# Optimization experiments

Measured on AMD Instinct MI355X. Metric: run time of the kernel, lower is better.

## Reference

```python
import jax, jax.numpy as jnp
import numpy as np

D_MODEL = 1024
N_HEADS = 16
N_GROUPS = 4
CONTEXT_LEN = 512
D_H = D_MODEL // N_HEADS          # 64
GROUP_SIZE = N_HEADS // N_GROUPS  # 4
B, S = 4, 2048


def setup_inputs() -> dict:
    key = jax.random.key(0)
    ks = jax.random.split(key, 9)
    s = 0.02
    return {
        "x": jax.random.normal(ks[0], (B, S, D_MODEL), dtype=jnp.float32),
        "Wq": jax.random.normal(ks[1], (D_MODEL, D_MODEL), dtype=jnp.float32) * s,
        "bq": jax.random.normal(ks[2], (D_MODEL,), dtype=jnp.float32) * s,
        "Wk": jax.random.normal(ks[3], (D_MODEL, N_GROUPS * D_H), dtype=jnp.float32) * s,
        "bk": jax.random.normal(ks[4], (N_GROUPS * D_H,), dtype=jnp.float32) * s,
        "Wv": jax.random.normal(ks[5], (D_MODEL, N_GROUPS * D_H), dtype=jnp.float32) * s,
        "bv": jax.random.normal(ks[6], (N_GROUPS * D_H,), dtype=jnp.float32) * s,
        "Wo": jax.random.normal(ks[7], (D_MODEL, D_MODEL), dtype=jnp.float32) * s,
        "bo": jax.random.normal(ks[8], (D_MODEL,), dtype=jnp.float32) * s,
    }


def reference(x, Wq, bq, Wk, bk, Wv, bv, Wo, bo):
    b, s = x.shape[0], x.shape[1]
    # Projections. q: [b, n_groups, group_size, s, d_h]; k/v: [b, n_groups, s, d_h]
    q = (x @ Wq + bq).reshape(b, s, N_GROUPS, GROUP_SIZE, D_H)
    q = jnp.transpose(q, (0, 2, 3, 1, 4))
    k = jnp.transpose((x @ Wk + bk).reshape(b, s, N_GROUPS, D_H), (0, 2, 1, 3))
    v = jnp.transpose((x @ Wv + bv).reshape(b, s, N_GROUPS, D_H), (0, 2, 1, 3))
    # Grouped scores (einsum broadcast == repeat_interleave of k over group_size)
    scores = jnp.einsum("bghqd,bgkd->bghqk", q, k) / jnp.sqrt(jnp.float32(D_H))
    # Sliding-window causal mask (cached_len == s when use_cache=False)
    i = jnp.arange(s)
    j = jnp.arange(s)
    upper = (i - CONTEXT_LEN)[:, None] >= j[None, :]   # too-old keys
    lower = i[:, None] < j[None, :]                    # future keys
    mask = upper | lower                               # [s, s]
    scores = jnp.where(mask, jnp.float32(-1e9), scores)
    att = jax.nn.softmax(scores, axis=-1)
    out = jnp.einsum("bghqk,bgkd->bghqd", att, v)      # [b, g, h, s, d_h]
    out = jnp.transpose(out, (0, 3, 1, 2, 4)).reshape(b, s, D_MODEL)
    return out @ Wo + bo
```

## Files before the change

### kernel.cpp

```cpp
#include <hip/hip_runtime.h>
#include <cstdint>
#include <cstddef>

typedef __attribute__((ext_vector_type(8))) short short8;
typedef __attribute__((ext_vector_type(4))) short short4v;
typedef __attribute__((ext_vector_type(4))) float f32x4;
typedef __attribute__((ext_vector_type(4))) unsigned short ushort4v;
typedef unsigned short ushort_t;

union Frag8 { short4v h[2]; short8 v; };
union PFrag { unsigned int w[4]; short8 v; };

__device__ __forceinline__ ushort_t f2bf(float f) {
  unsigned int u = __builtin_bit_cast(unsigned int, f);
  u += 0x7FFFu + ((u >> 16) & 1u);
  return (ushort_t)(u >> 16);
}

__device__ __forceinline__ void gload16(const void* g, void* l) {
  __builtin_amdgcn_global_load_lds(
      (const __attribute__((address_space(1))) unsigned int*)g,
      (__attribute__((address_space(3))) unsigned int*)l, 16, 0, 0);
}

__global__ void cast_x_kernel(const float* __restrict__ x, ushort_t* __restrict__ o) {
  int i = (blockIdx.x * 256 + threadIdx.x) * 4;
  const float4 v = *reinterpret_cast<const float4*>(x + i);
  ushort4v r = { f2bf(v.x), f2bf(v.y), f2bf(v.z), f2bf(v.w) };
  *reinterpret_cast<ushort4v*>(o + i) = r;
}

__global__ __launch_bounds__(256) void transpose_w_kernel(
    const float* __restrict__ Wq, const float* __restrict__ Wk,
    const float* __restrict__ Wv, const float* __restrict__ Wo,
    ushort_t* __restrict__ Wt) {
  __shared__ float tile[32][33];
  const int tn = blockIdx.x, tk = blockIdx.y;
  const int n0 = tn * 32;
  const float* W; int ldn, nloc;
  if      (n0 < 1024) { W = Wq; ldn = 1024; nloc = n0; }
  else if (n0 < 1280) { W = Wk; ldn = 256;  nloc = n0 - 1024; }
  else if (n0 < 1536) { W = Wv; ldn = 256;  nloc = n0 - 1280; }
  else                { W = Wo; ldn = 1024; nloc = n0 - 1536; }
  const int t = threadIdx.x;
  const int sr = t >> 3, sc = (t & 7) * 4;
  const float4 v = *reinterpret_cast<const float4*>(W + (size_t)(tk * 32 + sr) * ldn + nloc + sc);
  tile[sr][sc] = v.x; tile[sr][sc + 1] = v.y; tile[sr][sc + 2] = v.z; tile[sr][sc + 3] = v.w;
  __syncthreads();
  const int wr = t >> 3, wc = (t & 7) * 4;
  ushort4v o = { f2bf(tile[wc][wr]), f2bf(tile[wc + 1][wr]),
                 f2bf(tile[wc + 2][wr]), f2bf(tile[wc + 3][wr]) };
  *reinterpret_cast<ushort4v*>(Wt + (size_t)(n0 + wr) * 1024 + tk * 32 + wc) = o;
}

__global__ void prep_bias_kernel(const float* __restrict__ bq, const float* __restrict__ bk,
                                 const float* __restrict__ bv, float* __restrict__ bqkv) {
  int t = blockIdx.x * 256 + threadIdx.x;
  if (t < 1536) bqkv[t] = (t < 1024) ? bq[t] : (t < 1280) ? bk[t - 1024] : bv[t - 1280];
}

#define GEMM_IDS \
  const int tid = threadIdx.x;                        \
  const int w = tid >> 6, lane = tid & 63;            \
  const int wm = w >> 1, wn = w & 1;                  \
  const int g = lane >> 4, r16 = lane & 15;

#define GEMM_KLOOP(APTR, BPTR)                                                          \
  const f32x4 vzero = {0.f, 0.f, 0.f, 0.f};                                             \
  f32x4 acc[4][4];                                                                      \
  _Pragma("unroll") for (int i = 0; i < 4; ++i)                                         \
    _Pragma("unroll") for (int j = 0; j < 4; ++j) acc[i][j] = vzero;                    \
  auto stage = [&](int s, int k0) {                                                     \
    char* base = LdsB + s * 16384;                                                      \
    _Pragma("unroll") for (int i = 0; i < 2; ++i) {                                     \
      const int u = tid + i * 256;                                                      \
      const int row = u >> 2;                                                           \
      const int pu = (u & 3) ^ ((u >> 3) & 3);                                          \
      gload16((const char*)(APTR) + (size_t)(bm * 128 + row) * 2048 + k0 * 2 + pu * 16, \
              base + u * 16);                                                           \
    }                                                                                   \
    _Pragma("unroll") for (int i = 0; i < 2; ++i) {                                     \
      const int u = tid + i * 256;                                                      \
      const int row = u >> 2;                                                           \
      const int pu = (u & 3) ^ ((u >> 3) & 3);                                          \
      gload16((const char*)(BPTR) + (size_t)(bn * 128 + row) * 2048 + k0 * 2 + pu * 16, \
              base + 8192 + u * 16);                                                    \
    }                                                                                   \
  };                                                                                    \
  stage(0, 0);                                                                          \
  stage(1, 32);                                                                         \
  const int fsw = (g ^ ((r16 >> 1) & 3)) << 4;                                          \
  for (int t = 0; t < 32; ++t) {                                                        \
    if (t < 31) { asm volatile("s_waitcnt vmcnt(4) lgkmcnt(0)" ::: "memory"); }         \
    else        { asm volatile("s_waitcnt vmcnt(0) lgkmcnt(0)" ::: "memory"); }         \
    __builtin_amdgcn_s_barrier();                                                       \
    if (t + 2 < 32) stage((t + 2) % 3, (t + 2) * 32);                                   \
    const char* Ab = LdsB + (t % 3) * 16384;                                            \
    const char* Bb = Ab + 8192;                                                         \
    short8 af[4], bf[4];                                                                \
    _Pragma("unroll") for (int mi = 0; mi < 4; ++mi)                                    \
      af[mi] = *(const short8*)(Ab + (wm * 64 + mi * 16 + r16) * 64 + fsw);             \
    _Pragma("unroll") for (int ni = 0; ni < 4; ++ni)                                    \
      bf[ni] = *(const short8*)(Bb + (wn * 64 + ni * 16 + r16) * 64 + fsw);             \
    __builtin_amdgcn_s_setprio(1);                                                      \
    _Pragma("unroll") for (int mi = 0; mi < 4; ++mi)                                    \
      _Pragma("unroll") for (int ni = 0; ni < 4; ++ni)                                  \
        acc[mi][ni] = __builtin_amdgcn_mfma_f32_16x16x32_bf16(af[mi], bf[ni], acc[mi][ni], 0, 0, 0); \
    __builtin_amdgcn_s_setprio(0);                                                      \
  }

__global__ __launch_bounds__(256, 3) void gemm_qkv_kernel(
    const ushort_t* __restrict__ A, const ushort_t* __restrict__ Bt,
    const float* __restrict__ bias,
    ushort_t* __restrict__ Qb, ushort_t* __restrict__ Kb, ushort_t* __restrict__ Vt)
{
  __shared__ __align__(16) char LdsB[49152];
  const int xcd = blockIdx.x & 7, ii = blockIdx.x >> 3;
  const int bm = xcd * 8 + ii / 12, bn = ii % 12;
  GEMM_IDS
  GEMM_KLOOP(A, Bt)

  float bcol[4];
#pragma unroll
  for (int ni = 0; ni < 4; ++ni) bcol[ni] = bias[bn * 128 + wn * 64 + ni * 16 + r16];
  if (bn < 8) {
#pragma unroll
    for (int mi = 0; mi < 4; ++mi)
#pragma unroll
      for (int ni = 0; ni < 4; ++ni) {
        const int col = bn * 128 + wn * 64 + ni * 16 + r16;
#pragma unroll
        for (int rr = 0; rr < 4; ++rr) {
          const int row = bm * 128 + wm * 64 + mi * 16 + g * 4 + rr;
          Qb[(size_t)row * 1024 + col] = f2bf((acc[mi][ni][rr] + bcol[ni]) * 0.180336881f);
        }
      }
  } else if (bn < 10) {
#pragma unroll
    for (int mi = 0; mi < 4; ++mi)
#pragma unroll
      for (int ni = 0; ni < 4; ++ni) {
        const int c = bn * 128 + wn * 64 + ni * 16 + r16 - 1024;
        const int gi = c >> 6, dd = c & 63;
#pragma unroll
        for (int rr = 0; rr < 4; ++rr) {
          const int row = bm * 128 + wm * 64 + mi * 16 + g * 4 + rr;
          const int bb = row >> 11, s = row & 2047;
          Kb[((size_t)(bb * 4 + gi) * 2048 + s) * 64 + dd] = f2bf(acc[mi][ni][rr] + bcol[ni]);
        }
      }
  } else {
#pragma unroll
    for (int mi = 0; mi < 4; ++mi) {
      const int row0 = bm * 128 + wm * 64 + mi * 16 + g * 4;
      const int bb = row0 >> 11;
      const int s = row0 & 2047;
      const int pos = (s & ~31) + g * 8 + (mi & 1) * 4;
#pragma unroll
      for (int ni = 0; ni < 4; ++ni) {
        const int c = bn * 128 + wn * 64 + ni * 16 + r16 - 1280;
        const int gi = c >> 6, dd = c & 63;
        ushort4v pk;
#pragma unroll
        for (int rr = 0; rr < 4; ++rr) pk[rr] = f2bf(acc[mi][ni][rr] + bcol[ni]);
        *reinterpret_cast<ushort4v*>(Vt + ((size_t)(bb * 4 + gi) * 64 + dd) * 2048 + pos) = pk;
      }
    }
  }
}

__global__ __launch_bounds__(256, 2) void gemm_out_kernel(
    const ushort_t* __restrict__ A, const ushort_t* __restrict__ Bt,
    const float* __restrict__ bias, float* __restrict__ Cout)
{
  __shared__ __align__(16) char LdsB[49152];
  const int xcd = blockIdx.x & 7, ii = blockIdx.x >> 3;
  const int bm = xcd * 8 + (ii >> 3), bn = ii & 7;
  GEMM_IDS
  GEMM_KLOOP(A, Bt)

  float bcol[4];
#pragma unroll
  for (int ni = 0; ni < 4; ++ni) bcol[ni] = bias[bn * 128 + wn * 64 + ni * 16 + r16];
#pragma unroll
  for (int mi = 0; mi < 4; ++mi)
#pragma unroll
    for (int ni = 0; ni < 4; ++ni) {
      const int col = bn * 128 + wn * 64 + ni * 16 + r16;
#pragma unroll
      for (int rr = 0; rr < 4; ++rr) {
        const int row = bm * 128 + wm * 64 + mi * 16 + g * 4 + rr;
        Cout[(size_t)row * 1024 + col] = acc[mi][ni][rr] + bcol[ni];
      }
    }
}

__global__ __launch_bounds__(512, 2) void attn_kernel(
    const ushort_t* __restrict__ Qb, const ushort_t* __restrict__ Kb,
    const ushort_t* __restrict__ Vt, ushort_t* __restrict__ attout)
{
  __shared__ __align__(16) char KsB[24576];
  __shared__ __align__(16) char VsB[24576];
  const int fid = blockIdx.x;
  const int lo = fid & 7, hi = fid >> 3;
  const int qt = 31 - (hi & 31);
  const int gbsel = lo | ((hi >> 5) << 3);
  const int gg = gbsel & 3, b = gbsel >> 2;

  const int tid = threadIdx.x;
  const int w = tid >> 6, lane = tid & 63;
  const int hw = w & 3, qh = w >> 2;
  const int h = gg * 4 + hw;
  const int g = lane >> 4, r16 = lane & 15;
  const int q0w = qt * 64 + qh * 32;

  short8 qf[2][2];
#pragma unroll
  for (int qs = 0; qs < 2; ++qs) {
    const char* qptr = (const char*)Qb + ((size_t)(b * 2048 + q0w + qs * 16 + r16) * 1024 + h * 64) * 2;
#pragma unroll
    for (int dc = 0; dc < 2; ++dc)
      qf[qs][dc] = *(const short8*)(qptr + dc * 64 + g * 16);
  }

  const f32x4 vzero = {0.f, 0.f, 0.f, 0.f};
  f32x4 accO[2][4];
#pragma unroll
  for (int qs = 0; qs < 2; ++qs)
#pragma unroll
    for (int nt = 0; nt < 4; ++nt) accO[qs][nt] = vzero;
  float lsum[2] = {0.f, 0.f};

  const char* KbB = (const char*)Kb + (size_t)(b * 4 + gg) * 2048 * 128;
  const char* VtB = (const char*)Vt + (size_t)(b * 4 + gg) * 64 * 4096;

  const int kb0 = (qt >= 8) ? (qt * 64 - 512) : 0;
  const int NT = (qt * 64 + 64 - kb0) >> 6;

  const int srr = tid >> 3, spk = tid & 7;
  auto stage = [&](int buf, int kb) {
    gload16(KbB + (size_t)(kb + srr) * 128 + ((spk ^ (srr & 7)) << 4),
            KsB + buf * 8192 + tid * 16);
    gload16(VtB + (size_t)srr * 4096 + (size_t)kb * 2 + ((spk ^ (srr & 7)) << 4),
            VsB + buf * 8192 + tid * 16);
  };

  stage(0, kb0);
  if (NT > 1) stage(1, kb0 + 64);
  for (int t = 0; t < NT; ++t) {
    if (t < NT - 1) { asm volatile("s_waitcnt vmcnt(2) lgkmcnt(0)" ::: "memory"); }
    else            { asm volatile("s_waitcnt vmcnt(0) lgkmcnt(0)" ::: "memory"); }
    __builtin_amdgcn_s_barrier();
    if (t + 2 < NT) stage((t + 2) % 3, kb0 + (t + 2) * 64);
    const int kb = kb0 + t * 64;
    const char* Ks = KsB + (t % 3) * 8192;
    const char* Vs = VsB + (t % 3) * 8192;

    f32x4 st[2][4];
#pragma unroll
    for (int ki = 0; ki < 4; ++ki) {
      const int key = ki * 16 + r16;
      const int swz = key & 7;
      const short8 kf0 = *(const short8*)(Ks + key * 128 + ((g ^ swz) << 4));
      const short8 kf1 = *(const short8*)(Ks + key * 128 + (((4 + g) ^ swz) << 4));
#pragma unroll
      for (int qs = 0; qs < 2; ++qs) {
        st[qs][ki] = __builtin_amdgcn_mfma_f32_16x16x32_bf16(kf0, qf[qs][0], vzero, 0, 0, 0);
        st[qs][ki] = __builtin_amdgcn_mfma_f32_16x16x32_bf16(kf1, qf[qs][1], st[qs][ki], 0, 0, 0);
      }
    }

    const bool full = (kb >= q0w - 480) && (kb <= q0w - 63);
    PFrag pf[2][2];
    if (full) {
#pragma unroll
      for (int qs = 0; qs < 2; ++qs) {
#pragma unroll
        for (int ki = 0; ki < 4; ++ki)
#pragma unroll
          for (int r = 0; r < 4; ++r)
            st[qs][ki][r] = __builtin_amdgcn_exp2f(st[qs][ki][r]);
      }
    } else {
#pragma unroll
      for (int qs = 0; qs < 2; ++qs) {
        const int q = q0w + qs * 16 + r16;
#pragma unroll
        for (int ki = 0; ki < 4; ++ki)
#pragma unroll
          for (int r = 0; r < 4; ++r) {
            const int key = kb + ki * 16 + g * 4 + r;
            const bool valid = (key <= q) && (key + 512 > q);
            st[qs][ki][r] = __builtin_amdgcn_exp2f(valid ? st[qs][ki][r] : -INFINITY);
          }
      }
    }
#pragma unroll
    for (int qs = 0; qs < 2; ++qs) {
      float tk[4];
#pragma unroll
      for (int ki = 0; ki < 4; ++ki)
        tk[ki] = (st[qs][ki][0] + st[qs][ki][1]) + (st[qs][ki][2] + st[qs][ki][3]);
      lsum[qs] += (tk[0] + tk[1]) + (tk[2] + tk[3]);
#pragma unroll
      for (int c = 0; c < 2; ++c)
#pragma unroll
        for (int pr = 0; pr < 2; ++pr) {
          asm("v_cvt_pk_bf16_f32 %0, %1, %2"
              : "=v"(pf[qs][c].w[pr * 2])
              : "v"(st[qs][2 * c + pr][0]), "v"(st[qs][2 * c + pr][1]));
          asm("v_cvt_pk_bf16_f32 %0, %1, %2"
              : "=v"(pf[qs][c].w[pr * 2 + 1])
              : "v"(st[qs][2 * c + pr][2]), "v"(st[qs][2 * c + pr][3]));
        }
    }

#pragma unroll
    for (int c = 0; c < 2; ++c)
#pragma unroll
      for (int nt = 0; nt < 4; ++nt) {
        const int d = nt * 16 + r16;
        const short8 vf = *(const short8*)(Vs + d * 128 + (((c * 4 + g) ^ (d & 7)) << 4));
#pragma unroll
        for (int qs = 0; qs < 2; ++qs)
          accO[qs][nt] = __builtin_amdgcn_mfma_f32_16x16x32_bf16(pf[qs][c].v, vf, accO[qs][nt], 0, 0, 0);
      }
  }

#pragma unroll
  for (int qs = 0; qs < 2; ++qs) {
    float ts = lsum[qs];
    ts += __shfl_xor(ts, 16);
    ts += __shfl_xor(ts, 32);
    const float linv = 1.f / ts;
    float lq[4];
#pragma unroll
    for (int rr = 0; rr < 4; ++rr) lq[rr] = __shfl(linv, g * 4 + rr);
#pragma unroll
    for (int nt = 0; nt < 4; ++nt) {
      const int ocol = h * 64 + nt * 16 + r16;
#pragma unroll
      for (int rr = 0; rr < 4; ++rr) {
        const int orow = b * 2048 + q0w + qs * 16 + g * 4 + rr;
        attout[(size_t)orow * 1024 + ocol] = f2bf(accO[qs][nt][rr] * lq[rr]);
      }
    }
  }
}

extern "C" void kernel_launch(void* const* d_in, const int* in_sizes, int n_in,
                              void* d_out, int out_size, void* d_ws, size_t ws_size,
                              hipStream_t stream) {
  (void)in_sizes; (void)n_in; (void)out_size; (void)ws_size;
  const float* x  = (const float*)d_in[0];
  const float* Wq = (const float*)d_in[1];
  const float* bq = (const float*)d_in[2];
  const float* Wk = (const float*)d_in[3];
  const float* bk = (const float*)d_in[4];
  const float* Wv = (const float*)d_in[5];
  const float* bv = (const float*)d_in[6];
  const float* Wo = (const float*)d_in[7];
  const float* bo = (const float*)d_in[8];

  char* ws = (char*)d_ws;
  ushort_t* Qb   = (ushort_t*)(ws + 0);
  ushort_t* Kb   = (ushort_t*)(ws + 16777216);
  ushort_t* Vt   = (ushort_t*)(ws + 20971520);
  ushort_t* wt   = (ushort_t*)(ws + 25165824);
  float*    bqkv = (float*)   (ws + 30408704);
  ushort_t* xb   = (ushort_t*)(ws + 30416896);
  ushort_t* att  = (ushort_t*)(ws + 47194112);

  cast_x_kernel<<<8192, 256, 0, stream>>>(x, xb);
  transpose_w_kernel<<<dim3(80, 32), 256, 0, stream>>>(Wq, Wk, Wv, Wo, wt);
  prep_bias_kernel<<<6, 256, 0, stream>>>(bq, bk, bv, bqkv);
  gemm_qkv_kernel<<<768, 256, 0, stream>>>(xb, wt, bqkv, Qb, Kb, Vt);
  attn_kernel<<<512, 512, 0, stream>>>(Qb, Kb, Vt, att);
  gemm_out_kernel<<<512, 256, 0, stream>>>(att, wt + (size_t)1536 * 1024, bo, (float*)d_out);
}
```

Measured before the change: 104.0 us.

## Fuse fp32-to-bf16 cast of x into QKV GEMM A-tile loading

Removes the separate cast_x kernel and its bf16 intermediate buffer. The QKV GEMM now loads fp32 x rows into registers, converts them with packed bf16 conversion instructions, and writes swizzled tiles to LDS, software-pipelined alongside the async B-tile loads. This saves a launch and a full write/read of the bf16 copy of x, at the cost of doubled A-tile global traffic per GEMM block (read by 12 column blocks) and more registers and VALU work in the main loop. It also raises the occupancy hint of the output GEMM from 2 to 3 blocks per CU.

```diff
diff --git a/kernel.cpp b/kernel.cpp
--- a/kernel.cpp
+++ b/kernel.cpp
@@ -6,6 +6,7 @@
 typedef __attribute__((ext_vector_type(4))) short short4v;
 typedef __attribute__((ext_vector_type(4))) float f32x4;
 typedef __attribute__((ext_vector_type(4))) unsigned short ushort4v;
+typedef __attribute__((ext_vector_type(4))) unsigned int uint4v;
 typedef unsigned short ushort_t;
 
 union Frag8 { short4v h[2]; short8 v; };
@@ -23,11 +24,11 @@
       (__attribute__((address_space(3))) unsigned int*)l, 16, 0, 0);
 }
 
-__global__ void cast_x_kernel(const float* __restrict__ x, ushort_t* __restrict__ o) {
-  int i = (blockIdx.x * 256 + threadIdx.x) * 4;
-  const float4 v = *reinterpret_cast<const float4*>(x + i);
-  ushort4v r = { f2bf(v.x), f2bf(v.y), f2bf(v.z), f2bf(v.w) };
-  *reinterpret_cast<ushort4v*>(o + i) = r;
+__device__ __forceinline__ void cvt8(const float4& a, const float4& b, uint4v& o) {
+  asm("v_cvt_pk_bf16_f32 %0, %1, %2" : "=v"(o.x) : "v"(a.x), "v"(a.y));
+  asm("v_cvt_pk_bf16_f32 %0, %1, %2" : "=v"(o.y) : "v"(a.z), "v"(a.w));
+  asm("v_cvt_pk_bf16_f32 %0, %1, %2" : "=v"(o.z) : "v"(b.x), "v"(b.y));
+  asm("v_cvt_pk_bf16_f32 %0, %1, %2" : "=v"(o.w) : "v"(b.z), "v"(b.w));
 }
 
 __global__ __launch_bounds__(256) void transpose_w_kernel(
@@ -110,7 +111,7 @@
   }
 
 __global__ __launch_bounds__(256, 3) void gemm_qkv_kernel(
-    const ushort_t* __restrict__ A, const ushort_t* __restrict__ Bt,
+    const float* __restrict__ X, const ushort_t* __restrict__ Bt,
     const float* __restrict__ bias,
     ushort_t* __restrict__ Qb, ushort_t* __restrict__ Kb, ushort_t* __restrict__ Vt)
 {
@@ -118,7 +119,83 @@
   const int xcd = blockIdx.x & 7, ii = blockIdx.x >> 3;
   const int bm = xcd * 8 + ii / 12, bn = ii % 12;
   GEMM_IDS
-  GEMM_KLOOP(A, Bt)
+
+  const f32x4 vzero = {0.f, 0.f, 0.f, 0.f};
+  f32x4 acc[4][4];
+#pragma unroll
+  for (int i = 0; i < 4; ++i)
+#pragma unroll
+    for (int j = 0; j < 4; ++j) acc[i][j] = vzero;
+
+  const int arow = tid >> 1;
+  const int alu0 = (tid & 1) * 2;
+  const int asw  = (arow >> 1) & 3;
+  const float* aptr = X + (size_t)(bm * 128 + arow) * 1024 + alu0 * 8;
+  char* const awr = LdsB  + arow * 64;
+
+  auto issueA = [&](int k0, float4* r) {
+    const float* p = aptr + k0;
+#pragma unroll
+    for (int i = 0; i < 4; ++i) r[i] = *reinterpret_cast<const float4*>(p + i * 4);
+  };
+  auto issueB = [&](int s, int k0) {
+    char* base = LdsB + s * 16384 + 8192;
+#pragma unroll
+    for (int i = 0; i < 2; ++i) {
+      const int u = tid + i * 256;
+      const int row = u >> 2;
+      const int pu = (u & 3) ^ ((u >> 3) & 3);
+      gload16((const char*)Bt + (size_t)(bn * 128 + row) * 2048 + k0 * 2 + pu * 16,
+              base + u * 16);
+    }
+  };
+  auto writeA = [&](int s, const float4* r) {
+    char* base = awr + s * 16384;
+    uint4v p0, p1;
+    cvt8(r[0], r[1], p0);
+    cvt8(r[2], r[3], p1);
+    *reinterpret_cast<uint4v*>(base + ((alu0 ^ asw) << 4)) = p0;
+    *reinterpret_cast<uint4v*>(base + (((alu0 + 1) ^ asw) << 4)) = p1;
+  };
+
+  float4 rA0[4], rA1[4];
+  issueB(0, 0);  issueA(0, rA0);
+  issueB(1, 32); issueA(32, rA1);
+  asm volatile("s_waitcnt vmcnt(6)" ::: "memory");
+  writeA(0, rA0);
+
+  const int fsw = (g ^ ((r16 >> 1) & 3)) << 4;
+  auto iter = [&](int t, float4* rIssue, float4* rWrite) {
+    asm volatile("s_waitcnt lgkmcnt(0)" ::: "memory");
+    __builtin_amdgcn_s_barrier();
+    if (t + 2 < 32) { issueB((t + 2) % 3, (t + 2) * 32); issueA((t + 2) * 32, rIssue); }
+    const char* Ab = LdsB + (t % 3) * 16384;
+    const char* Bb = Ab + 8192;
+    short8 af[4], bf[4];
+#pragma unroll
+    for (int mi = 0; mi < 4; ++mi)
+      af[mi] = *(const short8*)(Ab + (wm * 64 + mi * 16 + r16) * 64 + fsw);
+#pragma unroll
+    for (int ni = 0; ni < 4; ++ni)
+      bf[ni] = *(const short8*)(Bb + (wn * 64 + ni * 16 + r16) * 64 + fsw);
+    __builtin_amdgcn_s_setprio(1);
+#pragma unroll
+    for (int mi = 0; mi < 4; ++mi)
+#pragma unroll
+      for (int ni = 0; ni < 4; ++ni)
+        acc[mi][ni] = __builtin_amdgcn_mfma_f32_16x16x32_bf16(af[mi], bf[ni], acc[mi][ni], 0, 0, 0);
+    __builtin_amdgcn_s_setprio(0);
+    __builtin_amdgcn_sched_barrier(0);
+    if (t + 1 < 32) {
+      if (t + 2 < 32) { asm volatile("s_waitcnt vmcnt(6)" ::: "memory"); }
+      else            { asm volatile("s_waitcnt vmcnt(0)" ::: "memory"); }
+      writeA((t + 1) % 3, rWrite);
+    }
+  };
+  for (int tt = 0; tt < 16; ++tt) {
+    iter(2 * tt,     rA0, rA1);
+    iter(2 * tt + 1, rA1, rA0);
+  }
 
   float bcol[4];
 #pragma unroll
@@ -169,7 +246,7 @@
   }
 }
 
-__global__ __launch_bounds__(256, 2) void gemm_out_kernel(
+__global__ __launch_bounds__(256, 3) void gemm_out_kernel(
     const ushort_t* __restrict__ A, const ushort_t* __restrict__ Bt,
     const float* __restrict__ bias, float* __restrict__ Cout)
 {
@@ -368,13 +445,11 @@
   ushort_t* Vt   = (ushort_t*)(ws + 20971520);
   ushort_t* wt   = (ushort_t*)(ws + 25165824);
   float*    bqkv = (float*)   (ws + 30408704);
-  ushort_t* xb   = (ushort_t*)(ws + 30416896);
   ushort_t* att  = (ushort_t*)(ws + 47194112);
 
-  cast_x_kernel<<<8192, 256, 0, stream>>>(x, xb);
   transpose_w_kernel<<<dim3(80, 32), 256, 0, stream>>>(Wq, Wk, Wv, Wo, wt);
   prep_bias_kernel<<<6, 256, 0, stream>>>(bq, bk, bv, bqkv);
-  gemm_qkv_kernel<<<768, 256, 0, stream>>>(xb, wt, bqkv, Qb, Kb, Vt);
+  gemm_qkv_kernel<<<768, 256, 0, stream>>>(x, wt, bqkv, Qb, Kb, Vt);
   attn_kernel<<<512, 512, 0, stream>>>(Qb, Kb, Vt, att);
   gemm_out_kernel<<<512, 256, 0, stream>>>(att, wt + (size_t)1536 * 1024, bo, (float*)d_out);
 }
```

Measured after the change: 106.7 us. +2.5%, slower.

## Process all four group heads per wave in attention; fold bias prep into transpose

Applied to the files above, without the earlier changes.

The attention kernel now gives each wave 16 queries across all 4 heads of a group, instead of 32 queries of one head. Each loaded K/V fragment is therefore reused across 4 heads, and the block covers 128 queries with half as many blocks. The bias-packing kernel is merged into the weight transpose kernel to drop one launch, and gemm_out's launch bounds request 3 blocks per CU. More accumulator and score registers per wave could lower occupancy, and fewer, larger attention blocks reduce the amount of parallelism.

```diff
diff --git a/kernel.cpp b/kernel.cpp
--- a/kernel.cpp
+++ b/kernel.cpp
@@ -8,7 +8,6 @@
 typedef __attribute__((ext_vector_type(4))) unsigned short ushort4v;
 typedef unsigned short ushort_t;
 
-union Frag8 { short4v h[2]; short8 v; };
 union PFrag { unsigned int w[4]; short8 v; };
 
 __device__ __forceinline__ ushort_t f2bf(float f) {
@@ -33,9 +32,15 @@
 __global__ __launch_bounds__(256) void transpose_w_kernel(
     const float* __restrict__ Wq, const float* __restrict__ Wk,
     const float* __restrict__ Wv, const float* __restrict__ Wo,
-    ushort_t* __restrict__ Wt) {
+    const float* __restrict__ bq, const float* __restrict__ bk,
+    const float* __restrict__ bv, ushort_t* __restrict__ Wt,
+    float* __restrict__ bqkv) {
   __shared__ float tile[32][33];
   const int tn = blockIdx.x, tk = blockIdx.y;
+  if (tk == 0) {
+    const int t = tn * 256 + threadIdx.x;
+    if (t < 1536) bqkv[t] = (t < 1024) ? bq[t] : (t < 1280) ? bk[t - 1024] : bv[t - 1280];
+  }
   const int n0 = tn * 32;
   const float* W; int ldn, nloc;
   if      (n0 < 1024) { W = Wq; ldn = 1024; nloc = n0; }
@@ -51,12 +56,6 @@
   ushort4v o = { f2bf(tile[wc][wr]), f2bf(tile[wc + 1][wr]),
                  f2bf(tile[wc + 2][wr]), f2bf(tile[wc + 3][wr]) };
   *reinterpret_cast<ushort4v*>(Wt + (size_t)(n0 + wr) * 1024 + tk * 32 + wc) = o;
-}
-
-__global__ void prep_bias_kernel(const float* __restrict__ bq, const float* __restrict__ bk,
-                                 const float* __restrict__ bv, float* __restrict__ bqkv) {
-  int t = blockIdx.x * 256 + threadIdx.x;
-  if (t < 1536) bqkv[t] = (t < 1024) ? bq[t] : (t < 1280) ? bk[t - 1024] : bv[t - 1280];
 }
 
 #define GEMM_IDS \
@@ -169,7 +168,7 @@
   }
 }
 
-__global__ __launch_bounds__(256, 2) void gemm_out_kernel(
+__global__ __launch_bounds__(256, 3) void gemm_out_kernel(
     const ushort_t* __restrict__ A, const ushort_t* __restrict__ Bt,
     const float* __restrict__ bias, float* __restrict__ Cout)
 {
@@ -203,39 +202,38 @@
   __shared__ __align__(16) char VsB[24576];
   const int fid = blockIdx.x;
   const int lo = fid & 7, hi = fid >> 3;
-  const int qt = 31 - (hi & 31);
-  const int gbsel = lo | ((hi >> 5) << 3);
-  const int gg = gbsel & 3, b = gbsel >> 2;
+  const int qt = 15 - (hi & 15);
+  const int gb = lo | ((hi >> 4) << 3);
+  const int gg = gb & 3, b = gb >> 2;
 
   const int tid = threadIdx.x;
   const int w = tid >> 6, lane = tid & 63;
-  const int hw = w & 3, qh = w >> 2;
-  const int h = gg * 4 + hw;
   const int g = lane >> 4, r16 = lane & 15;
-  const int q0w = qt * 64 + qh * 32;
-
-  short8 qf[2][2];
-#pragma unroll
-  for (int qs = 0; qs < 2; ++qs) {
-    const char* qptr = (const char*)Qb + ((size_t)(b * 2048 + q0w + qs * 16 + r16) * 1024 + h * 64) * 2;
+  const int q0w = qt * 128 + w * 16;
+
+  short8 qf[4][2];
+#pragma unroll
+  for (int hh = 0; hh < 4; ++hh) {
+    const int h = gg * 4 + hh;
+    const char* qptr = (const char*)Qb + ((size_t)(b * 2048 + q0w + r16) * 1024 + h * 64) * 2;
 #pragma unroll
     for (int dc = 0; dc < 2; ++dc)
-      qf[qs][dc] = *(const short8*)(qptr + dc * 64 + g * 16);
+      qf[hh][dc] = *(const short8*)(qptr + dc * 64 + g * 16);
   }
 
   const f32x4 vzero = {0.f, 0.f, 0.f, 0.f};
-  f32x4 accO[2][4];
-#pragma unroll
-  for (int qs = 0; qs < 2; ++qs)
-#pragma unroll
-    for (int nt = 0; nt < 4; ++nt) accO[qs][nt] = vzero;
-  float lsum[2] = {0.f, 0.f};
+  f32x4 accO[4][4];
+#pragma unroll
+  for (int hh = 0; hh < 4; ++hh)
+#pragma unroll
+    for (int nt = 0; nt < 4; ++nt) accO[hh][nt] = vzero;
+  float lsum[4] = {0.f, 0.f, 0.f, 0.f};
 
   const char* KbB = (const char*)Kb + (size_t)(b * 4 + gg) * 2048 * 128;
   const char* VtB = (const char*)Vt + (size_t)(b * 4 + gg) * 64 * 4096;
 
-  const int kb0 = (qt >= 8) ? (qt * 64 - 512) : 0;
-  const int NT = (qt * 64 + 64 - kb0) >> 6;
+  const int kb0 = (qt >= 4) ? (qt * 128 - 512) : 0;
+  const int NT = (qt * 128 + 128 - kb0) >> 6;
 
   const int srr = tid >> 3, spk = tid & 7;
   auto stage = [&](int buf, int kb) {
@@ -256,7 +254,7 @@
     const char* Ks = KsB + (t % 3) * 8192;
     const char* Vs = VsB + (t % 3) * 8192;
 
-    f32x4 st[2][4];
+    f32x4 st[4][4];
 #pragma unroll
     for (int ki = 0; ki < 4; ++ki) {
       const int key = ki * 16 + r16;
@@ -264,54 +262,52 @@
       const short8 kf0 = *(const short8*)(Ks + key * 128 + ((g ^ swz) << 4));
       const short8 kf1 = *(const short8*)(Ks + key * 128 + (((4 + g) ^ swz) << 4));
 #pragma unroll
-      for (int qs = 0; qs < 2; ++qs) {
-        st[qs][ki] = __builtin_amdgcn_mfma_f32_16x16x32_bf16(kf0, qf[qs][0], vzero, 0, 0, 0);
-        st[qs][ki] = __builtin_amdgcn_mfma_f32_16x16x32_bf16(kf1, qf[qs][1], st[qs][ki], 0, 0, 0);
-      }
-    }
-
-    const bool full = (kb >= q0w - 480) && (kb <= q0w - 63);
-    PFrag pf[2][2];
+      for (int hh = 0; hh < 4; ++hh) {
+        st[hh][ki] = __builtin_amdgcn_mfma_f32_16x16x32_bf16(kf0, qf[hh][0], vzero, 0, 0, 0);
+        st[hh][ki] = __builtin_amdgcn_mfma_f32_16x16x32_bf16(kf1, qf[hh][1], st[hh][ki], 0, 0, 0);
+      }
+    }
+
+    const bool full = (kb >= q0w - 496) && (kb <= q0w - 63);
     if (full) {
 #pragma unroll
-      for (int qs = 0; qs < 2; ++qs) {
+      for (int hh = 0; hh < 4; ++hh)
 #pragma unroll
         for (int ki = 0; ki < 4; ++ki)
 #pragma unroll
           for (int r = 0; r < 4; ++r)
-            st[qs][ki][r] = __builtin_amdgcn_exp2f(st[qs][ki][r]);
-      }
+            st[hh][ki][r] = __builtin_amdgcn_exp2f(st[hh][ki][r]);
     } else {
-#pragma unroll
-      for (int qs = 0; qs < 2; ++qs) {
-        const int q = q0w + qs * 16 + r16;
-#pragma unroll
-        for (int ki = 0; ki < 4; ++ki)
-#pragma unroll
-          for (int r = 0; r < 4; ++r) {
-            const int key = kb + ki * 16 + g * 4 + r;
-            const bool valid = (key <= q) && (key + 512 > q);
-            st[qs][ki][r] = __builtin_amdgcn_exp2f(valid ? st[qs][ki][r] : -INFINITY);
-          }
-      }
-    }
-#pragma unroll
-    for (int qs = 0; qs < 2; ++qs) {
+      const int q = q0w + r16;
+#pragma unroll
+      for (int ki = 0; ki < 4; ++ki)
+#pragma unroll
+        for (int r = 0; r < 4; ++r) {
+          const int key = kb + ki * 16 + g * 4 + r;
+          const bool valid = (key <= q) && (key + 512 > q);
+#pragma unroll
+          for (int hh = 0; hh < 4; ++hh)
+            st[hh][ki][r] = __builtin_amdgcn_exp2f(valid ? st[hh][ki][r] : -INFINITY);
+        }
+    }
+    PFrag pf[4][2];
+#pragma unroll
+    for (int hh = 0; hh < 4; ++hh) {
       float tk[4];
 #pragma unroll
       for (int ki = 0; ki < 4; ++ki)
-        tk[ki] = (st[qs][ki][0] + st[qs][ki][1]) + (st[qs][ki][2] + st[qs][ki][3]);
-      lsum[qs] += (tk[0] + tk[1]) + (tk[2] + tk[3]);
+        tk[ki] = (st[hh][ki][0] + st[hh][ki][1]) + (st[hh][ki][2] + st[hh][ki][3]);
+      lsum[hh] += (tk[0] + tk[1]) + (tk[2] + tk[3]);
 #pragma unroll
       for (int c = 0; c < 2; ++c)
 #pragma unroll
         for (int pr = 0; pr < 2; ++pr) {
           asm("v_cvt_pk_bf16_f32 %0, %1, %2"
-              : "=v"(pf[qs][c].w[pr * 2])
-              : "v"(st[qs][2 * c + pr][0]), "v"(st[qs][2 * c + pr][1]));
+              : "=v"(pf[hh][c].w[pr * 2])
+              : "v"(st[hh][2 * c + pr][0]), "v"(st[hh][2 * c + pr][1]));
           asm("v_cvt_pk_bf16_f32 %0, %1, %2"
-              : "=v"(pf[qs][c].w[pr * 2 + 1])
-              : "v"(st[qs][2 * c + pr][2]), "v"(st[qs][2 * c + pr][3]));
+              : "=v"(pf[hh][c].w[pr * 2 + 1])
+              : "v"(st[hh][2 * c + pr][2]), "v"(st[hh][2 * c + pr][3]));
         }
     }
 
@@ -322,27 +318,28 @@
         const int d = nt * 16 + r16;
         const short8 vf = *(const short8*)(Vs + d * 128 + (((c * 4 + g) ^ (d & 7)) << 4));
 #pragma unroll
-        for (int qs = 0; qs < 2; ++qs)
-          accO[qs][nt] = __builtin_amdgcn_mfma_f32_16x16x32_bf16(pf[qs][c].v, vf, accO[qs][nt], 0, 0, 0);
-      }
-  }
-
-#pragma unroll
-  for (int qs = 0; qs < 2; ++qs) {
-    float ts = lsum[qs];
+        for (int hh = 0; hh < 4; ++hh)
+          accO[hh][nt] = __builtin_amdgcn_mfma_f32_16x16x32_bf16(pf[hh][c].v, vf, accO[hh][nt], 0, 0, 0);
+      }
+  }
+
+#pragma unroll
+  for (int hh = 0; hh < 4; ++hh) {
+    float ts = lsum[hh];
     ts += __shfl_xor(ts, 16);
     ts += __shfl_xor(ts, 32);
     const float linv = 1.f / ts;
     float lq[4];
 #pragma unroll
     for (int rr = 0; rr < 4; ++rr) lq[rr] = __shfl(linv, g * 4 + rr);
+    const int h = gg * 4 + hh;
 #pragma unroll
     for (int nt = 0; nt < 4; ++nt) {
       const int ocol = h * 64 + nt * 16 + r16;
 #pragma unroll
       for (int rr = 0; rr < 4; ++rr) {
-        const int orow = b * 2048 + q0w + qs * 16 + g * 4 + rr;
-        attout[(size_t)orow * 1024 + ocol] = f2bf(accO[qs][nt][rr] * lq[rr]);
+        const int orow = b * 2048 + q0w + g * 4 + rr;
+        attout[(size_t)orow * 1024 + ocol] = f2bf(accO[hh][nt][rr] * lq[rr]);
       }
     }
   }
@@ -372,9 +369,8 @@
   ushort_t* att  = (ushort_t*)(ws + 47194112);
 
   cast_x_kernel<<<8192, 256, 0, stream>>>(x, xb);
-  transpose_w_kernel<<<dim3(80, 32), 256, 0, stream>>>(Wq, Wk, Wv, Wo, wt);
-  prep_bias_kernel<<<6, 256, 0, stream>>>(bq, bk, bv, bqkv);
+  transpose_w_kernel<<<dim3(80, 32), 256, 0, stream>>>(Wq, Wk, Wv, Wo, bq, bk, bv, wt, bqkv);
   gemm_qkv_kernel<<<768, 256, 0, stream>>>(xb, wt, bqkv, Qb, Kb, Vt);
-  attn_kernel<<<512, 512, 0, stream>>>(Qb, Kb, Vt, att);
+  attn_kernel<<<256, 512, 0, stream>>>(Qb, Kb, Vt, att);
   gemm_out_kernel<<<512, 256, 0, stream>>>(att, wt + (size_t)1536 * 1024, bo, (float*)d_out);
 }
```

Measured after the change: 102.9 us. About the same (-1.1%).
